# Kernel optimization log

Measured on AMD Instinct MI355X. Metric: run time of the kernel, lower is better.

Reference implementation:

```python
import jax, jax.numpy as jnp
import numpy as np

K = 6            # kmer length
NF = 8192        # n_filters (> 4**K so kmer_params has shape (NF, 4, K))
M = 4 ** K       # 4096 kmers
B = 1024         # batch


def setup_inputs() -> dict:
    key = jax.random.key(0)
    k1, k2 = jax.random.split(key)
    freq = jax.random.uniform(k1, (B, M), dtype=jnp.float32)          # kmer frequencies (B, 4^k)
    kmer_params = jax.random.normal(k2, (NF, 4, K), dtype=jnp.float32)
    temperature = jnp.ones((1,), dtype=jnp.float32)
    # base-4 digits of arange(4^k), most-significant first == itertools.product order
    pos = 4 ** jnp.arange(K - 1, -1, -1)
    kmer_idcs = ((jnp.arange(M)[:, None] // pos[None, :]) % 4).astype(jnp.int32)  # (M, K)
    return {"freq": freq, "kmer_params": kmer_params,
            "temperature": temperature, "kmer_idcs": kmer_idcs}


def reference(freq, kmer_params, temperature, kmer_idcs):
    k = kmer_params.shape[-1]
    # matches[f, i] = sum_j kmer_params[f, kmer_idcs[i, j], j]
    # Advanced indexing broadcasts (M, k) indices against arange(k): result (F, M, k).
    # This replaces torch's expand-to-(F, M, 1, k) + gather + squeeze + sum(-1).
    matches = kmer_params[:, kmer_idcs, jnp.arange(k)].sum(axis=-1)   # (F, M)
    probs = jax.nn.softmax(matches / temperature, axis=1)             # softmax over kmers
    pooled = freq @ probs.T                                           # (B, F)
    profile = pooled / pooled.sum(axis=1, keepdims=True)
    return profile
```

## Files before the change

kernel.cpp:

```cpp
#include <hip/hip_runtime.h>


typedef __bf16  bf16x8 __attribute__((ext_vector_type(8)));
typedef float   f32x4  __attribute__((ext_vector_type(4)));
typedef short   short8v __attribute__((ext_vector_type(8)));

#define GLD16(gp, lp)                                                          \
  __builtin_amdgcn_global_load_lds(                                            \
      (const __attribute__((address_space(1))) void*)(gp),                     \
      (__attribute__((address_space(3))) void*)(lp), 16, 0, 0)

__device__ __forceinline__ short f2bf(float x) {
  unsigned u = __float_as_uint(x);
  unsigned r = (u + 0x7fffu + ((u >> 16) & 1u)) >> 16;
  return (short)r;
}

__device__ __forceinline__ float wave_max(float v) {
  #pragma unroll
  for (int off = 32; off; off >>= 1) v = fmaxf(v, __shfl_xor(v, off, 64));
  return v;
}
__device__ __forceinline__ float wave_sum(float v) {
  #pragma unroll
  for (int off = 32; off; off >>= 1) v += __shfl_xor(v, off, 64);
  return v;
}

__global__ __launch_bounds__(256) void cast_kernel(const float* __restrict__ in,
                                                   short* __restrict__ out) {
  int idx = blockIdx.x * 256 + threadIdx.x;
  float4 v = ((const float4*)in)[idx];
  short4 o;
  o.x = f2bf(v.x); o.y = f2bf(v.y); o.z = f2bf(v.z); o.w = f2bf(v.w);
  ((short4*)out)[idx] = o;
}

__global__ __launch_bounds__(256) void probs_kernel(const float* __restrict__ kp,
                                                    const float* __restrict__ temp,
                                                    short* __restrict__ probs) {
  const int f = blockIdx.x;
  const int t = threadIdx.x;
  const int lane = t & 63, wave = t >> 6;

  __shared__ float P[24];
  __shared__ float Thi[64], Tlo[64];
  __shared__ float redA[4], redB[4];

  if (t < 24) P[t] = kp[f * 24 + t];
  __syncthreads();
  if (t < 64) {
    Thi[t] = P[((t >> 4) & 3) * 6 + 0] + P[((t >> 2) & 3) * 6 + 1] + P[(t & 3) * 6 + 2];
    Tlo[t] = P[((t >> 4) & 3) * 6 + 3] + P[((t >> 2) & 3) * 6 + 4] + P[(t & 3) * 6 + 5];
  }
  __syncthreads();

  const float hi = Thi[t >> 2];
  const int lo0 = (t & 3) * 16;
  float m[16];
  float mx = -1e30f;
  #pragma unroll
  for (int s = 0; s < 16; s++) {
    m[s] = hi + Tlo[lo0 + s];
    mx = fmaxf(mx, m[s]);
  }
  float wmx = wave_max(mx);
  if (lane == 0) redA[wave] = wmx;
  __syncthreads();
  mx = fmaxf(fmaxf(redA[0], redA[1]), fmaxf(redA[2], redA[3]));

  const float invT = 1.0f / temp[0];
  float e[16];
  float lsum = 0.0f;
  #pragma unroll
  for (int s = 0; s < 16; s++) {
    e[s] = __expf((m[s] - mx) * invT);
    lsum += e[s];
  }
  float wsum = wave_sum(lsum);
  if (lane == 0) redB[wave] = wsum;
  __syncthreads();
  float tot = (redB[0] + redB[1]) + (redB[2] + redB[3]);
  float inv = 1.0f / tot;

  short8v* prow = (short8v*)(probs + (size_t)f * 4096 + t * 16);
  short8v o0, o1;
  #pragma unroll
  for (int s = 0; s < 8; s++) { o0[s] = f2bf(e[s] * inv); o1[s] = f2bf(e[s + 8] * inv); }
  prow[0] = o0;
  prow[1] = o1;
}

__global__ __launch_bounds__(256) void gemm_kernel(const short* __restrict__ A,
                                                   const short* __restrict__ Bm,
                                                   float* __restrict__ C) {
  __shared__ short As[128 * 64];
  __shared__ short Bs[128 * 64];

  const int t = threadIdx.x;
  const int lane = t & 63, wave = t >> 6;
  const int quad = lane >> 4, l16 = lane & 15;
  const int m0 = blockIdx.y * 128;
  const int n0 = blockIdx.x * 128;
  const int wm = (wave & 1) * 64, wn = (wave >> 1) * 64;

  f32x4 acc[4][4];
  #pragma unroll
  for (int i = 0; i < 4; i++)
    #pragma unroll
    for (int j = 0; j < 4; j++) acc[i][j] = (f32x4){0.f, 0.f, 0.f, 0.f};

  const int lane_row = lane >> 3;
  const int src_col = ((lane & 7) ^ lane_row) * 8;
  const int sw = l16 & 7;

  for (int kt = 0; kt < 64; kt++) {
    const int kofs = kt * 64;
    __syncthreads();
    #pragma unroll
    for (int c = 0; c < 4; c++) {
      const int chunk = wave * 4 + c;
      const int row = chunk * 8 + lane_row;
      GLD16(A  + (m0 + row) * 4096 + kofs + src_col, &As[chunk * 512 + lane * 8]);
      GLD16(Bm + (n0 + row) * 4096 + kofs + src_col, &Bs[chunk * 512 + lane * 8]);
    }
    __syncthreads();

    #pragma unroll
    for (int ks = 0; ks < 2; ks++) {
      const int pcol = ((ks * 4 + quad) ^ sw) * 8;
      bf16x8 a[4], b[4];
      #pragma unroll
      for (int i = 0; i < 4; i++)
        a[i] = *(const bf16x8*)&As[(wm + i * 16 + l16) * 64 + pcol];
      #pragma unroll
      for (int j = 0; j < 4; j++)
        b[j] = *(const bf16x8*)&Bs[(wn + j * 16 + l16) * 64 + pcol];
      #pragma unroll
      for (int i = 0; i < 4; i++)
        #pragma unroll
        for (int j = 0; j < 4; j++)
          acc[i][j] = __builtin_amdgcn_mfma_f32_16x16x32_bf16(a[i], b[j], acc[i][j], 0, 0, 0);
    }
  }

  #pragma unroll
  for (int i = 0; i < 4; i++) {
    #pragma unroll
    for (int r = 0; r < 4; r++) {
      const int brow = m0 + wm + i * 16 + quad * 4 + r;
      float* crow = C + brow * 8192 + n0 + wn + l16;
      #pragma unroll
      for (int j = 0; j < 4; j++) crow[j * 16] = acc[i][j][r];
    }
  }
}

__global__ __launch_bounds__(256) void norm_kernel(float* __restrict__ out) {
  const int b = blockIdx.x;
  const int t = threadIdx.x;
  const int lane = t & 63, wave = t >> 6;
  __shared__ float red[4];

  float4* row = (float4*)(out + b * 8192);
  float4 v[8];
  float s = 0.0f;
  #pragma unroll
  for (int q = 0; q < 8; q++) {
    v[q] = row[q * 256 + t];
    s += (v[q].x + v[q].y) + (v[q].z + v[q].w);
  }
  float ws = wave_sum(s);
  if (lane == 0) red[wave] = ws;
  __syncthreads();
  float tot = (red[0] + red[1]) + (red[2] + red[3]);
  float inv = 1.0f / tot;
  #pragma unroll
  for (int q = 0; q < 8; q++) {
    v[q].x *= inv; v[q].y *= inv; v[q].z *= inv; v[q].w *= inv;
    row[q * 256 + t] = v[q];
  }
}

extern "C" void kernel_launch(void* const* d_in, const int* in_sizes, int n_in,
                              void* d_out, int out_size, void* d_ws, size_t ws_size,
                              hipStream_t stream) {
  const float* freq    = (const float*)d_in[0];
  const float* kparams = (const float*)d_in[1];
  const float* temp    = (const float*)d_in[2];

  float* out = (float*)d_out;

  short* probs = (short*)d_ws;
  short* freqb = probs + (size_t)8192 * 4096;

  cast_kernel <<<4096, 256, 0, stream>>>(freq, freqb);
  probs_kernel<<<8192, 256, 0, stream>>>(kparams, temp, probs);
  gemm_kernel <<<dim3(64, 8), 256, 0, stream>>>(freqb, probs, out);
  norm_kernel <<<1024, 256, 0, stream>>>(out);
}
```

Measured before the change: 182.2 us.

## Factor softmax into rank-one hi/lo exp tables and generate B operand in GEMM

```diff
diff --git a/kernel.cpp b/kernel.cpp
--- a/kernel.cpp
+++ b/kernel.cpp
@@ -3,7 +3,6 @@
 
 typedef __bf16  bf16x8 __attribute__((ext_vector_type(8)));
 typedef float   f32x4  __attribute__((ext_vector_type(4)));
-typedef short   short8v __attribute__((ext_vector_type(8)));
 
 #define GLD16(gp, lp)                                                          \
   __builtin_amdgcn_global_load_lds(                                            \
@@ -36,66 +35,32 @@
   ((short4*)out)[idx] = o;
 }
 
-__global__ __launch_bounds__(256) void probs_kernel(const float* __restrict__ kp,
-                                                    const float* __restrict__ temp,
-                                                    short* __restrict__ probs) {
-  const int f = blockIdx.x;
+__global__ __launch_bounds__(256) void tables_kernel(const float* __restrict__ kp,
+                                                     const float* __restrict__ temp,
+                                                     float* __restrict__ E1t,
+                                                     float* __restrict__ E2) {
   const int t = threadIdx.x;
   const int lane = t & 63, wave = t >> 6;
-
-  __shared__ float P[24];
-  __shared__ float Thi[64], Tlo[64];
-  __shared__ float redA[4], redB[4];
-
-  if (t < 24) P[t] = kp[f * 24 + t];
-  __syncthreads();
-  if (t < 64) {
-    Thi[t] = P[((t >> 4) & 3) * 6 + 0] + P[((t >> 2) & 3) * 6 + 1] + P[(t & 3) * 6 + 2];
-    Tlo[t] = P[((t >> 4) & 3) * 6 + 3] + P[((t >> 2) & 3) * 6 + 4] + P[(t & 3) * 6 + 5];
-  }
-  __syncthreads();
-
-  const float hi = Thi[t >> 2];
-  const int lo0 = (t & 3) * 16;
-  float m[16];
-  float mx = -1e30f;
-  #pragma unroll
-  for (int s = 0; s < 16; s++) {
-    m[s] = hi + Tlo[lo0 + s];
-    mx = fmaxf(mx, m[s]);
-  }
-  float wmx = wave_max(mx);
-  if (lane == 0) redA[wave] = wmx;
-  __syncthreads();
-  mx = fmaxf(fmaxf(redA[0], redA[1]), fmaxf(redA[2], redA[3]));
-
+  const int f = blockIdx.x * 4 + wave;
+  const float* P = kp + f * 24;
+  const int d0 = (lane >> 4) & 3, d1 = (lane >> 2) & 3, d2 = lane & 3;
+  const float thi = P[d0 * 6 + 0] + P[d1 * 6 + 1] + P[d2 * 6 + 2];
+  const float tlo = P[d0 * 6 + 3] + P[d1 * 6 + 4] + P[d2 * 6 + 5];
+  const float mxhi = wave_max(thi), mxlo = wave_max(tlo);
   const float invT = 1.0f / temp[0];
-  float e[16];
-  float lsum = 0.0f;
-  #pragma unroll
-  for (int s = 0; s < 16; s++) {
-    e[s] = __expf((m[s] - mx) * invT);
-    lsum += e[s];
-  }
-  float wsum = wave_sum(lsum);
-  if (lane == 0) redB[wave] = wsum;
-  __syncthreads();
-  float tot = (redB[0] + redB[1]) + (redB[2] + redB[3]);
-  float inv = 1.0f / tot;
-
-  short8v* prow = (short8v*)(probs + (size_t)f * 4096 + t * 16);
-  short8v o0, o1;
-  #pragma unroll
-  for (int s = 0; s < 8; s++) { o0[s] = f2bf(e[s] * inv); o1[s] = f2bf(e[s + 8] * inv); }
-  prow[0] = o0;
-  prow[1] = o1;
+  const float e1 = __expf((thi - mxhi) * invT);
+  const float e2 = __expf((tlo - mxlo) * invT);
+  const float s1 = wave_sum(e1), s2 = wave_sum(e2);
+  const float invZ = 1.0f / (s1 * s2);
+  E1t[lane * 8192 + f] = e1 * invZ;
+  E2[(size_t)f * 64 + lane] = e2;
 }
 
-__global__ __launch_bounds__(256) void gemm_kernel(const short* __restrict__ A,
-                                                   const short* __restrict__ Bm,
-                                                   float* __restrict__ C) {
+__global__ __launch_bounds__(256, 2) void gemm_kernel(const short* __restrict__ A,
+                                                      const float* __restrict__ E1t,
+                                                      const float* __restrict__ E2,
+                                                      float* __restrict__ C) {
   __shared__ short As[128 * 64];
-  __shared__ short Bs[128 * 64];
 
   const int t = threadIdx.x;
   const int lane = t & 63, wave = t >> 6;
@@ -110,37 +75,68 @@
     #pragma unroll
     for (int j = 0; j < 4; j++) acc[i][j] = (f32x4){0.f, 0.f, 0.f, 0.f};
 
+  int nrow[4];
+  #pragma unroll
+  for (int j = 0; j < 4; j++) nrow[j] = n0 + wn + j * 16 + l16;
+  float4 e2a[4][2], e2b[4][2];
+  #pragma unroll
+  for (int j = 0; j < 4; j++)
+    #pragma unroll
+    for (int ks = 0; ks < 2; ks++) {
+      const float* p = E2 + (size_t)nrow[j] * 64 + (ks * 4 + quad) * 8;
+      e2a[j][ks] = *(const float4*)p;
+      e2b[j][ks] = *(const float4*)(p + 4);
+    }
+
   const int lane_row = lane >> 3;
   const int src_col = ((lane & 7) ^ lane_row) * 8;
   const int sw = l16 & 7;
 
   for (int kt = 0; kt < 64; kt++) {
     const int kofs = kt * 64;
+    float e1v[4];
+    #pragma unroll
+    for (int j = 0; j < 4; j++) e1v[j] = E1t[kt * 8192 + nrow[j]];
+
     __syncthreads();
     #pragma unroll
     for (int c = 0; c < 4; c++) {
       const int chunk = wave * 4 + c;
       const int row = chunk * 8 + lane_row;
-      GLD16(A  + (m0 + row) * 4096 + kofs + src_col, &As[chunk * 512 + lane * 8]);
-      GLD16(Bm + (n0 + row) * 4096 + kofs + src_col, &Bs[chunk * 512 + lane * 8]);
+      GLD16(A + (m0 + row) * 4096 + kofs + src_col, &As[chunk * 512 + lane * 8]);
     }
     __syncthreads();
+
+    bf16x8 b[2][4];
+    #pragma unroll
+    for (int j = 0; j < 4; j++)
+      #pragma unroll
+      for (int ks = 0; ks < 2; ks++) {
+        const float s = e1v[j];
+        bf16x8 bb;
+        bb[0] = (__bf16)(s * e2a[j][ks].x);
+        bb[1] = (__bf16)(s * e2a[j][ks].y);
+        bb[2] = (__bf16)(s * e2a[j][ks].z);
+        bb[3] = (__bf16)(s * e2a[j][ks].w);
+        bb[4] = (__bf16)(s * e2b[j][ks].x);
+        bb[5] = (__bf16)(s * e2b[j][ks].y);
+        bb[6] = (__bf16)(s * e2b[j][ks].z);
+        bb[7] = (__bf16)(s * e2b[j][ks].w);
+        b[ks][j] = bb;
+      }
 
     #pragma unroll
     for (int ks = 0; ks < 2; ks++) {
       const int pcol = ((ks * 4 + quad) ^ sw) * 8;
-      bf16x8 a[4], b[4];
+      bf16x8 a[4];
       #pragma unroll
       for (int i = 0; i < 4; i++)
         a[i] = *(const bf16x8*)&As[(wm + i * 16 + l16) * 64 + pcol];
       #pragma unroll
-      for (int j = 0; j < 4; j++)
-        b[j] = *(const bf16x8*)&Bs[(wn + j * 16 + l16) * 64 + pcol];
-      #pragma unroll
       for (int i = 0; i < 4; i++)
         #pragma unroll
         for (int j = 0; j < 4; j++)
-          acc[i][j] = __builtin_amdgcn_mfma_f32_16x16x32_bf16(a[i], b[j], acc[i][j], 0, 0, 0);
+          acc[i][j] = __builtin_amdgcn_mfma_f32_16x16x32_bf16(a[i], b[ks][j], acc[i][j], 0, 0, 0);
     }
   }
 
@@ -149,7 +145,7 @@
     #pragma unroll
     for (int r = 0; r < 4; r++) {
       const int brow = m0 + wm + i * 16 + quad * 4 + r;
-      float* crow = C + brow * 8192 + n0 + wn + l16;
+      float* crow = C + (size_t)brow * 8192 + n0 + wn + l16;
       #pragma unroll
       for (int j = 0; j < 4; j++) crow[j * 16] = acc[i][j][r];
     }
@@ -162,7 +158,7 @@
   const int lane = t & 63, wave = t >> 6;
   __shared__ float red[4];
 
-  float4* row = (float4*)(out + b * 8192);
+  float4* row = (float4*)(out + (size_t)b * 8192);
   float4 v[8];
   float s = 0.0f;
   #pragma unroll
@@ -191,11 +187,12 @@
 
   float* out = (float*)d_out;
 
-  short* probs = (short*)d_ws;
-  short* freqb = probs + (size_t)8192 * 4096;
+  short* freqb = (short*)d_ws;
+  float* E1t   = (float*)(freqb + (size_t)1024 * 4096);
+  float* E2    = E1t + (size_t)64 * 8192;
 
-  cast_kernel <<<4096, 256, 0, stream>>>(freq, freqb);
-  probs_kernel<<<8192, 256, 0, stream>>>(kparams, temp, probs);
-  gemm_kernel <<<dim3(64, 8), 256, 0, stream>>>(freqb, probs, out);
-  norm_kernel <<<1024, 256, 0, stream>>>(out);
+  cast_kernel  <<<4096, 256, 0, stream>>>(freq, freqb);
+  tables_kernel<<<2048, 256, 0, stream>>>(kparams, temp, E1t, E2);
+  gemm_kernel  <<<dim3(64, 8), 256, 0, stream>>>(freqb, E1t, E2, out);
+  norm_kernel  <<<1024, 256, 0, stream>>>(out);
 }
```

New measurement: 165.0 us. 1.1x faster.
